# Optimization experiments

Measured on AMD Instinct MI355X. Metric: run time of the kernel, lower is better.

Reference implementation:

```python
import jax, jax.numpy as jnp
import numpy as np

B, S, H, DK = 8, 2048, 1024, 64


def setup_inputs() -> dict:
    key = jax.random.key(0)
    ks = jax.random.split(key, 8)
    x = jax.random.normal(ks[0], (B, S, H), dtype=jnp.float32)
    # padding at the tail: positions >= length are pad (True)
    lengths = jax.random.randint(ks[1], (B,), S // 2, S + 1)
    padding_mask = jnp.arange(S)[None, :] >= lengths[:, None]  # [B,S] bool, True = pad
    sc = 1.0 / np.sqrt(H)
    Wq = jax.random.normal(ks[2], (H, DK), dtype=jnp.float32) * sc
    Wk = jax.random.normal(ks[3], (H, DK), dtype=jnp.float32) * sc
    Wv = jax.random.normal(ks[4], (H, DK), dtype=jnp.float32) * sc
    bq = jnp.zeros((DK,), dtype=jnp.float32)
    bk = jnp.zeros((DK,), dtype=jnp.float32)
    bv = jnp.zeros((DK,), dtype=jnp.float32)
    return {"x": x, "padding_mask": padding_mask, "Wq": Wq, "bq": bq,
            "Wk": Wk, "bk": bk, "Wv": Wv, "bv": bv}


def reference(x, padding_mask, Wq, bq, Wk, bk, Wv, bv):
    # Single-head attention, dropout_pe = 0 (identity), masking=True (causal).
    d_k = Wq.shape[-1]
    Q = jnp.einsum('bsh,hd->bsd', x, Wq) + bq
    K = jnp.einsum('bsh,hd->bsd', x, Wk) + bk
    V = jnp.einsum('bsh,hd->bsd', x, Wv) + bv
    scores = jnp.einsum('bqd,bkd->bqk', Q, K) / jnp.sqrt(jnp.asarray(d_k, x.dtype))
    neg_inf = jnp.finfo(scores.dtype).min
    # padding mask over keys: [B,1,S]
    scores = jnp.where(padding_mask[:, None, :], neg_inf, scores)
    # causal mask: strictly upper triangular is disallowed
    seq = scores.shape[-1]
    causal = jnp.triu(jnp.ones((seq, seq), dtype=bool), k=1)
    scores = jnp.where(causal[None, :, :], neg_inf, scores)
    W = jax.nn.softmax(scores, axis=-1)
    # zero out attention rows for padded query positions: [B,S,1]
    W = jnp.where(padding_mask[:, :, None], 0.0, W)
    return jnp.einsum('bqk,bkd->bqd', W, V)
```

## Files before the change

### kernel.cpp

```cpp
#include <hip/hip_runtime.h>
#include <hip/hip_bf16.h>

#define NB 8
#define SEQ 2048
#define HD 1024
#define DK 64

#define QSCALE 0.1803368801111244f
#define FIXMAX2 11.541560327111708f

typedef __attribute__((ext_vector_type(4))) float f32x4;
typedef __attribute__((ext_vector_type(8))) short bf16x8;
typedef __attribute__((ext_vector_type(4))) unsigned short u16x4;

#define LDS_BARRIER() asm volatile("s_waitcnt lgkmcnt(0)\n\ts_barrier" ::: "memory")

__device__ __forceinline__ short f2bf(float f) {
    union { float f; unsigned u; } v; v.f = f;
    unsigned r = v.u + 0x7fffu + ((v.u >> 16) & 1u);
    return (short)(r >> 16);
}
__device__ __forceinline__ float fexp2(float x) {
#if __has_builtin(__builtin_amdgcn_exp2f)
    return __builtin_amdgcn_exp2f(x);
#else
    return exp2f(x);
#endif
}
__device__ __forceinline__ short bf16lo(float f) {
    unsigned r;
    asm("v_cvt_pk_bf16_f32 %0, %1, %1" : "=v"(r) : "v"(f));
    return (short)r;
}
__device__ __forceinline__ bf16x8 pack8(f32x4 v0, f32x4 v1) {
    union { bf16x8 v; __hip_bfloat162 h[4]; } u;
    u.h[0] = __float22bfloat162_rn(make_float2(v0[0], v0[1]));
    u.h[1] = __float22bfloat162_rn(make_float2(v0[2], v0[3]));
    u.h[2] = __float22bfloat162_rn(make_float2(v1[0], v1[1]));
    u.h[3] = __float22bfloat162_rn(make_float2(v1[2], v1[3]));
    return u.v;
}

__global__ void prep_kernel(const unsigned* __restrict__ mask,
                            const float* __restrict__ Wq, const float* __restrict__ Wk,
                            const float* __restrict__ Wv,
                            int* __restrict__ lengths, short* __restrict__ Wp) {
    if (blockIdx.x < 768) {
        int idx = blockIdx.x * 256 + threadIdx.x;
        int j = idx & 7, lane = (idx >> 3) & 63;
        int slot = idx >> 9;
        int fr = slot % 3, q2 = slot / 3;
        int kh = q2 & 1, cg = (q2 >> 1) & 3, kbg = q2 >> 3;
        int g = lane >> 4, c = lane & 15;
        int n = cg * 3 + fr;
        int m = n >> 2, colm = (n & 3) * 16 + c;
        int k = kbg * 64 + kh * 32 + g * 8 + j;
        const float* W = (m == 0) ? Wq : (m == 1) ? Wk : Wv;
        Wp[idx] = f2bf(W[(size_t)k * DK + colm]);
        return;
    }
    __shared__ int sdet;
    __shared__ int scnt;
    int b = blockIdx.x - 768, t = threadIdx.x;
    if (t == 0) { sdet = 0; scnt = 0; }
    __syncthreads();
    int det = 0;
    for (int i = t; i < 4096; i += 256) {
        unsigned w = mask[i];
        if (w > 1u && w != 0x3F800000u) det = 1;
    }
    if (det) atomicOr(&sdet, 1);
    __syncthreads();
    int cnt = 0;
    if (sdet) {
        const unsigned char* m8 = (const unsigned char*)mask;
        for (int s = t; s < SEQ; s += 256) cnt += (m8[b * SEQ + s] == 0) ? 1 : 0;
    } else {
        for (int s = t; s < SEQ; s += 256) cnt += (mask[b * SEQ + s] == 0u) ? 1 : 0;
    }
    atomicAdd(&scnt, cnt);
    __syncthreads();
    if (t == 0) lengths[b] = scnt;
}

__global__ __launch_bounds__(256) void qkv_kernel(
    const float* __restrict__ x,
    const float* __restrict__ bq, const float* __restrict__ bk, const float* __restrict__ bv,
    const short* __restrict__ Wp,
    short* __restrict__ Q, short* __restrict__ K, short* __restrict__ Vt) {
    __shared__ short xs[2][32][64];
    int t = threadIdx.x;
    int cg = t >> 6, lane = t & 63;
    int g = lane >> 4, c = lane & 15;
    int r0 = blockIdx.x * 32;
    int bb = r0 >> 11, sbase = r0 & (SEQ - 1);

    int srow = t >> 3, ch = t & 7;
    const float* xsrc = x + (size_t)(r0 + srow) * HD + ch * 8;
    short* wbase = &xs[0][0][0];
    int wo = srow * 64 + ((ch ^ (srow & 7)) << 3);

    const short* wpw = Wp + (size_t)cg * 3072 + (size_t)lane * 8;

    f32x4 z = {0.f, 0.f, 0.f, 0.f};
    f32x4 acc[2][3];
    #pragma unroll
    for (int rf = 0; rf < 2; rf++)
        #pragma unroll
        for (int fr = 0; fr < 3; fr++) acc[rf][fr] = z;

    {
        f32x4 x0 = *(const f32x4*)xsrc;
        f32x4 x1 = *(const f32x4*)(xsrc + 4);
        *(bf16x8*)(wbase + wo) = pack8(x0, x1);
    }
    bf16x8 Bc[2][3];
    #pragma unroll
    for (int kh = 0; kh < 2; kh++)
        #pragma unroll
        for (int fr = 0; fr < 3; fr++)
            Bc[kh][fr] = *(const bf16x8*)(wpw + kh * 1536 + fr * 512);
    f32x4 nxA0 = *(const f32x4*)(xsrc + 64);
    f32x4 nxA1 = *(const f32x4*)(xsrc + 68);
    LDS_BARRIER();

    const short* rbase0 = &xs[0][0][0] + c * 64;
    #pragma unroll
    for (int kbg = 0; kbg < 16; kbg++) {
        int cur = kbg & 1;
        f32x4 nxB0, nxB1;
        bf16x8 Bn[2][3];
        if (kbg < 14) {
            const float* p = xsrc + (kbg + 2) * 64;
            nxB0 = *(const f32x4*)p;
            nxB1 = *(const f32x4*)(p + 4);
        }
        if (kbg < 15) {
            #pragma unroll
            for (int kh = 0; kh < 2; kh++)
                #pragma unroll
                for (int fr = 0; fr < 3; fr++)
                    Bn[kh][fr] = *(const bf16x8*)(wpw + (kbg + 1) * 12288 + kh * 1536 + fr * 512);
        }
        bf16x8 Af[2][2];
        #pragma unroll
        for (int rf = 0; rf < 2; rf++)
            #pragma unroll
            for (int kh = 0; kh < 2; kh++)
                Af[rf][kh] = *(const bf16x8*)(rbase0 + cur * 2048 + rf * 1024
                                              + (((kh * 4 + g) ^ (c & 7)) << 3));
        #pragma unroll
        for (int kh = 0; kh < 2; kh++)
            #pragma unroll
            for (int fr = 0; fr < 3; fr++)
                #pragma unroll
                for (int rf = 0; rf < 2; rf++)
                    acc[rf][fr] = __builtin_amdgcn_mfma_f32_16x16x32_bf16(Af[rf][kh], Bc[kh][fr], acc[rf][fr], 0, 0, 0);
        if (kbg < 15) {
            *(bf16x8*)(wbase + (cur ^ 1) * 2048 + wo) = pack8(nxA0, nxA1);
            #pragma unroll
            for (int kh = 0; kh < 2; kh++)
                #pragma unroll
                for (int fr = 0; fr < 3; fr++) Bc[kh][fr] = Bn[kh][fr];
        }
        if (kbg < 14) { nxA0 = nxB0; nxA1 = nxB1; }
        LDS_BARRIER();
    }

    #pragma unroll
    for (int rf = 0; rf < 2; rf++)
        #pragma unroll
        for (int fr = 0; fr < 3; fr++) {
            int n = cg * 3 + fr;
            int m = n >> 2, colm = (n & 3) * 16 + c;
            const float* bias = (m == 0) ? bq : (m == 1) ? bk : bv;
            float bv_ = bias[colm];
            if (m == 2) {
                u16x4 pk;
                #pragma unroll
                for (int j = 0; j < 4; j++) pk[j] = (unsigned short)f2bf(acc[rf][fr][j] + bv_);
                int srw = sbase + rf * 16 + 4 * g;
                *(u16x4*)(Vt + (size_t)bb * DK * SEQ + (size_t)colm * SEQ + srw) = pk;
            } else {
                #pragma unroll
                for (int j = 0; j < 4; j++) {
                    int row = r0 + rf * 16 + 4 * g + j;
                    float s = acc[rf][fr][j] + bv_;
                    if (m == 0) Q[(size_t)row * DK + colm] = f2bf(s * QSCALE);
                    else        K[(size_t)row * DK + colm] = f2bf(s);
                }
            }
        }
}

__global__ __launch_bounds__(512) void attn_kernel(
    const short* __restrict__ Q, const short* __restrict__ K_, const short* __restrict__ Vt,
    const int* __restrict__ lengths, float* __restrict__ out) {
    __shared__ float macc[8][32][66];
    __shared__ float ll[8][32];
    short* plds = (short*)&macc[0][0][0];

    int bid = blockIdx.x;
    int b = bid & 7;
    int qt = 63 - (bid >> 3);
    int len = lengths[b];
    int qbase = qt * 32;
    int t = threadIdx.x;
    int w = t >> 6, lane = t & 63;
    int g = lane >> 4, c = lane & 15;

    if (qbase >= len) {
        int row = t >> 4, col0 = (t & 15) * 4;
        f32x4 zz = {0.f, 0.f, 0.f, 0.f};
        *(f32x4*)(out + ((size_t)b * SEQ + qbase + row) * DK + col0) = zz;
        return;
    }

    int kend = min(len, qbase + 32);
    int ntiles = (kend + 63) >> 6;
    const short* Qb = Q + ((size_t)b * SEQ + qbase) * DK;
    const short* Kb = K_ + (size_t)b * SEQ * DK;
    const short* Vb = Vt + (size_t)b * DK * SEQ;

    bf16x8 qa[2][2];
    #pragma unroll
    for (int f = 0; f < 2; f++)
        #pragma unroll
        for (int kh = 0; kh < 2; kh++)
            qa[f][kh] = *(const bf16x8*)(Qb + (f * 16 + c) * DK + kh * 32 + g * 8);

    int rowcap[2][4];
    #pragma unroll
    for (int f = 0; f < 2; f++)
        #pragma unroll
        for (int j = 0; j < 4; j++)
            rowcap[f][j] = min(qbase + f * 16 + 4 * g + j, len - 1);

    f32x4 z = {0.f, 0.f, 0.f, 0.f};
    f32x4 acc[2][4];
    float l_r[2][4];
    #pragma unroll
    for (int f = 0; f < 2; f++) {
        #pragma unroll
        for (int n = 0; n < 4; n++) acc[f][n] = z;
        #pragma unroll
        for (int j = 0; j < 4; j++) l_r[f][j] = 0.f;
    }

    short* pldsw = plds + w * 2240;

    for (int tt = w; tt < ntiles; tt += 8) {
        int kb = tt * 64;
        bf16x8 kh0[2][2], kh1[2][2];
        #pragma unroll
        for (int kt = 0; kt < 2; kt++) {
            const short* kp = Kb + (size_t)(kb + kt * 16 + c) * DK + g * 8;
            kh0[kt][0] = *(const bf16x8*)kp;
            kh0[kt][1] = *(const bf16x8*)(kp + 32);
        }
        #pragma unroll
        for (int kt = 0; kt < 2; kt++) {
            const short* kp = Kb + (size_t)(kb + 32 + kt * 16 + c) * DK + g * 8;
            kh1[kt][0] = *(const bf16x8*)kp;
            kh1[kt][1] = *(const bf16x8*)(kp + 32);
        }
        f32x4 sf[2][4];
        __builtin_amdgcn_s_setprio(1);
        #pragma unroll
        for (int kt = 0; kt < 2; kt++)
            #pragma unroll
            for (int f = 0; f < 2; f++) {
                f32x4 t0 = __builtin_amdgcn_mfma_f32_16x16x32_bf16(qa[f][0], kh0[kt][0], z, 0, 0, 0);
                sf[f][kt] = __builtin_amdgcn_mfma_f32_16x16x32_bf16(qa[f][1], kh0[kt][1], t0, 0, 0, 0);
            }
        #pragma unroll
        for (int kt = 0; kt < 2; kt++)
            #pragma unroll
            for (int f = 0; f < 2; f++) {
                f32x4 t0 = __builtin_amdgcn_mfma_f32_16x16x32_bf16(qa[f][0], kh1[kt][0], z, 0, 0, 0);
                sf[f][kt + 2] = __builtin_amdgcn_mfma_f32_16x16x32_bf16(qa[f][1], kh1[kt][1], t0, 0, 0, 0);
            }
        __builtin_amdgcn_s_setprio(0);
        #pragma unroll
        for (int kt = 0; kt < 4; kt++) {
            int key = kb + kt * 16 + c;
            #pragma unroll
            for (int f = 0; f < 2; f++)
                #pragma unroll
                for (int j = 0; j < 4; j++) {
                    float s = (key > rowcap[f][j]) ? -1e30f : sf[f][kt][j];
                    float p = fexp2(s - FIXMAX2);
                    sf[f][kt][j] = p;
                    l_r[f][j] += p;
                }
        }
        #pragma unroll
        for (int f = 0; f < 2; f++)
            #pragma unroll
            for (int kt = 0; kt < 4; kt++)
                #pragma unroll
                for (int j = 0; j < 4; j++)
                    pldsw[f * 1120 + (4 * g + j) * 70 + kt * 16 + c] = bf16lo(sf[f][kt][j]);
        bf16x8 pa[2][2];
        #pragma unroll
        for (int f = 0; f < 2; f++) {
            pa[f][0] = *(const bf16x8*)(pldsw + f * 1120 + c * 70 + g * 8);
            pa[f][1] = *(const bf16x8*)(pldsw + f * 1120 + c * 70 + 32 + g * 8);
        }
        #pragma unroll
        for (int n = 0; n < 4; n++) {
            const short* vp = Vb + (size_t)(n * 16 + c) * SEQ + kb + g * 8;
            bf16x8 v0 = *(const bf16x8*)vp;
            bf16x8 v1 = *(const bf16x8*)(vp + 32);
            __builtin_amdgcn_s_setprio(1);
            #pragma unroll
            for (int f = 0; f < 2; f++) {
                acc[f][n] = __builtin_amdgcn_mfma_f32_16x16x32_bf16(pa[f][0], v0, acc[f][n], 0, 0, 0);
                acc[f][n] = __builtin_amdgcn_mfma_f32_16x16x32_bf16(pa[f][1], v1, acc[f][n], 0, 0, 0);
            }
            __builtin_amdgcn_s_setprio(0);
        }
    }

    #pragma unroll
    for (int d = 1; d < 16; d <<= 1)
        #pragma unroll
        for (int f = 0; f < 2; f++)
            #pragma unroll
            for (int j = 0; j < 4; j++) l_r[f][j] += __shfl_xor(l_r[f][j], d);

    __syncthreads();
    #pragma unroll
    for (int f = 0; f < 2; f++)
        #pragma unroll
        for (int n = 0; n < 4; n++)
            #pragma unroll
            for (int j = 0; j < 4; j++)
                macc[w][f * 16 + 4 * g + j][n * 16 + c] = acc[f][n][j];
    if (c == 0) {
        #pragma unroll
        for (int f = 0; f < 2; f++)
            #pragma unroll
            for (int j = 0; j < 4; j++)
                ll[w][f * 16 + 4 * g + j] = l_r[f][j];
    }
    __syncthreads();
    {
        int row = t >> 4, seg = t & 15;
        int r = qbase + row;
        float* op = out + ((size_t)b * SEQ + r) * DK + seg * 4;
        float o[4] = {0.f, 0.f, 0.f, 0.f};
        if (r < len) {
            float L = 0.f;
            #pragma unroll
            for (int wv = 0; wv < 8; wv++) L += ll[wv][row];
            #pragma unroll
            for (int wv = 0; wv < 8; wv++)
                #pragma unroll
                for (int i = 0; i < 4; i++) o[i] += macc[wv][row][seg * 4 + i];
            float inv = 1.f / L;
            #pragma unroll
            for (int i = 0; i < 4; i++) o[i] *= inv;
        }
        #pragma unroll
        for (int i = 0; i < 4; i++) op[i] = o[i];
    }
}

extern "C" void kernel_launch(void* const* d_in, const int* in_sizes, int n_in,
                              void* d_out, int out_size, void* d_ws, size_t ws_size,
                              hipStream_t stream) {
    const float* x  = (const float*)d_in[0];
    const unsigned* mask = (const unsigned*)d_in[1];
    const float* Wq = (const float*)d_in[2];
    const float* bq = (const float*)d_in[3];
    const float* Wk = (const float*)d_in[4];
    const float* bk = (const float*)d_in[5];
    const float* Wv = (const float*)d_in[6];
    const float* bv = (const float*)d_in[7];
    float* out = (float*)d_out;

    char* ws = (char*)d_ws;
    int*   lengths = (int*)ws;
    short* Wp = (short*)(ws + 256);
    short* Q  = (short*)(ws + 393472);
    short* K  = (short*)(ws + 2490624);
    short* Vt = (short*)(ws + 4587776);

    hipLaunchKernelGGL(prep_kernel, dim3(776), dim3(256), 0, stream, mask, Wq, Wk, Wv, lengths, Wp);
    hipLaunchKernelGGL(qkv_kernel, dim3(512), dim3(256), 0, stream,
                       x, bq, bk, bv, Wp, Q, K, Vt);
    hipLaunchKernelGGL(attn_kernel, dim3(NB * 64), dim3(512), 0, stream,
                       Q, K, Vt, lengths, out);
}
```

Measured before the change: 54.79 us.

## Split attention work across waves by query half and key-tile stride

Each wave now handles one 16-row query half (f = w&1) and every fourth key tile, instead of both query halves and every eighth key tile. This halves per-wave register state (accumulators, Q fragments, scores) and the LDS used for the final reduction, and the reduction now sums over 4 waves rather than 8. In exchange, each K/V tile is loaded by two waves instead of one, which adds global/L2 traffic, and fewer waves share each query's key range. The output store is also switched to a single vector write.

```diff
diff --git a/kernel.cpp b/kernel.cpp
--- a/kernel.cpp
+++ b/kernel.cpp
@@ -196,8 +196,8 @@
 __global__ __launch_bounds__(512) void attn_kernel(
     const short* __restrict__ Q, const short* __restrict__ K_, const short* __restrict__ Vt,
     const int* __restrict__ lengths, float* __restrict__ out) {
-    __shared__ float macc[8][32][66];
-    __shared__ float ll[8][32];
+    __shared__ float macc[8][16][66];
+    __shared__ float ll[8][16];
     short* plds = (short*)&macc[0][0][0];
 
     int bid = blockIdx.x;
@@ -208,6 +208,7 @@
     int t = threadIdx.x;
     int w = t >> 6, lane = t & 63;
     int g = lane >> 4, c = lane & 15;
+    int f = w & 1, sq = w >> 1;
 
     if (qbase >= len) {
         int row = t >> 4, col0 = (t & 15) * 4;
@@ -218,38 +219,26 @@
 
     int kend = min(len, qbase + 32);
     int ntiles = (kend + 63) >> 6;
-    const short* Qb = Q + ((size_t)b * SEQ + qbase) * DK;
+    const short* Qb = Q + ((size_t)b * SEQ + qbase + f * 16) * DK;
     const short* Kb = K_ + (size_t)b * SEQ * DK;
     const short* Vb = Vt + (size_t)b * DK * SEQ;
 
-    bf16x8 qa[2][2];
-    #pragma unroll
-    for (int f = 0; f < 2; f++)
-        #pragma unroll
-        for (int kh = 0; kh < 2; kh++)
-            qa[f][kh] = *(const bf16x8*)(Qb + (f * 16 + c) * DK + kh * 32 + g * 8);
-
-    int rowcap[2][4];
-    #pragma unroll
-    for (int f = 0; f < 2; f++)
-        #pragma unroll
-        for (int j = 0; j < 4; j++)
-            rowcap[f][j] = min(qbase + f * 16 + 4 * g + j, len - 1);
+    bf16x8 qa[2];
+    qa[0] = *(const bf16x8*)(Qb + c * DK + g * 8);
+    qa[1] = *(const bf16x8*)(Qb + c * DK + 32 + g * 8);
+
+    int rowcap[4];
+    #pragma unroll
+    for (int j = 0; j < 4; j++)
+        rowcap[j] = min(qbase + f * 16 + 4 * g + j, len - 1);
 
     f32x4 z = {0.f, 0.f, 0.f, 0.f};
-    f32x4 acc[2][4];
-    float l_r[2][4];
-    #pragma unroll
-    for (int f = 0; f < 2; f++) {
-        #pragma unroll
-        for (int n = 0; n < 4; n++) acc[f][n] = z;
-        #pragma unroll
-        for (int j = 0; j < 4; j++) l_r[f][j] = 0.f;
-    }
-
-    short* pldsw = plds + w * 2240;
-
-    for (int tt = w; tt < ntiles; tt += 8) {
+    f32x4 acc[4] = {z, z, z, z};
+    float l_r[4] = {0.f, 0.f, 0.f, 0.f};
+
+    short* pldsw = plds + w * 1120;
+
+    for (int tt = sq; tt < ntiles; tt += 4) {
         int kb = tt * 64;
         bf16x8 kh0[2][2], kh1[2][2];
         #pragma unroll
@@ -264,60 +253,45 @@
             kh1[kt][0] = *(const bf16x8*)kp;
             kh1[kt][1] = *(const bf16x8*)(kp + 32);
         }
-        f32x4 sf[2][4];
+        f32x4 sf[4];
         __builtin_amdgcn_s_setprio(1);
         #pragma unroll
-        for (int kt = 0; kt < 2; kt++)
-            #pragma unroll
-            for (int f = 0; f < 2; f++) {
-                f32x4 t0 = __builtin_amdgcn_mfma_f32_16x16x32_bf16(qa[f][0], kh0[kt][0], z, 0, 0, 0);
-                sf[f][kt] = __builtin_amdgcn_mfma_f32_16x16x32_bf16(qa[f][1], kh0[kt][1], t0, 0, 0, 0);
-            }
-        #pragma unroll
-        for (int kt = 0; kt < 2; kt++)
-            #pragma unroll
-            for (int f = 0; f < 2; f++) {
-                f32x4 t0 = __builtin_amdgcn_mfma_f32_16x16x32_bf16(qa[f][0], kh1[kt][0], z, 0, 0, 0);
-                sf[f][kt + 2] = __builtin_amdgcn_mfma_f32_16x16x32_bf16(qa[f][1], kh1[kt][1], t0, 0, 0, 0);
-            }
+        for (int kt = 0; kt < 2; kt++) {
+            f32x4 t0 = __builtin_amdgcn_mfma_f32_16x16x32_bf16(qa[0], kh0[kt][0], z, 0, 0, 0);
+            sf[kt] = __builtin_amdgcn_mfma_f32_16x16x32_bf16(qa[1], kh0[kt][1], t0, 0, 0, 0);
+        }
+        #pragma unroll
+        for (int kt = 0; kt < 2; kt++) {
+            f32x4 t0 = __builtin_amdgcn_mfma_f32_16x16x32_bf16(qa[0], kh1[kt][0], z, 0, 0, 0);
+            sf[kt + 2] = __builtin_amdgcn_mfma_f32_16x16x32_bf16(qa[1], kh1[kt][1], t0, 0, 0, 0);
+        }
         __builtin_amdgcn_s_setprio(0);
         #pragma unroll
         for (int kt = 0; kt < 4; kt++) {
             int key = kb + kt * 16 + c;
             #pragma unroll
-            for (int f = 0; f < 2; f++)
-                #pragma unroll
-                for (int j = 0; j < 4; j++) {
-                    float s = (key > rowcap[f][j]) ? -1e30f : sf[f][kt][j];
-                    float p = fexp2(s - FIXMAX2);
-                    sf[f][kt][j] = p;
-                    l_r[f][j] += p;
-                }
-        }
-        #pragma unroll
-        for (int f = 0; f < 2; f++)
-            #pragma unroll
-            for (int kt = 0; kt < 4; kt++)
-                #pragma unroll
-                for (int j = 0; j < 4; j++)
-                    pldsw[f * 1120 + (4 * g + j) * 70 + kt * 16 + c] = bf16lo(sf[f][kt][j]);
-        bf16x8 pa[2][2];
-        #pragma unroll
-        for (int f = 0; f < 2; f++) {
-            pa[f][0] = *(const bf16x8*)(pldsw + f * 1120 + c * 70 + g * 8);
-            pa[f][1] = *(const bf16x8*)(pldsw + f * 1120 + c * 70 + 32 + g * 8);
-        }
+            for (int j = 0; j < 4; j++) {
+                float s = (key > rowcap[j]) ? -1e30f : sf[kt][j];
+                float p = fexp2(s - FIXMAX2);
+                sf[kt][j] = p;
+                l_r[j] += p;
+            }
+        }
+        #pragma unroll
+        for (int kt = 0; kt < 4; kt++)
+            #pragma unroll
+            for (int j = 0; j < 4; j++)
+                pldsw[(4 * g + j) * 70 + kt * 16 + c] = bf16lo(sf[kt][j]);
+        bf16x8 pa0 = *(const bf16x8*)(pldsw + c * 70 + g * 8);
+        bf16x8 pa1 = *(const bf16x8*)(pldsw + c * 70 + 32 + g * 8);
         #pragma unroll
         for (int n = 0; n < 4; n++) {
             const short* vp = Vb + (size_t)(n * 16 + c) * SEQ + kb + g * 8;
             bf16x8 v0 = *(const bf16x8*)vp;
             bf16x8 v1 = *(const bf16x8*)(vp + 32);
             __builtin_amdgcn_s_setprio(1);
-            #pragma unroll
-            for (int f = 0; f < 2; f++) {
-                acc[f][n] = __builtin_amdgcn_mfma_f32_16x16x32_bf16(pa[f][0], v0, acc[f][n], 0, 0, 0);
-                acc[f][n] = __builtin_amdgcn_mfma_f32_16x16x32_bf16(pa[f][1], v1, acc[f][n], 0, 0, 0);
-            }
+            acc[n] = __builtin_amdgcn_mfma_f32_16x16x32_bf16(pa0, v0, acc[n], 0, 0, 0);
+            acc[n] = __builtin_amdgcn_mfma_f32_16x16x32_bf16(pa1, v1, acc[n], 0, 0, 0);
             __builtin_amdgcn_s_setprio(0);
         }
     }
@@ -325,45 +299,38 @@
     #pragma unroll
     for (int d = 1; d < 16; d <<= 1)
         #pragma unroll
-        for (int f = 0; f < 2; f++)
-            #pragma unroll
-            for (int j = 0; j < 4; j++) l_r[f][j] += __shfl_xor(l_r[f][j], d);
-
-    __syncthreads();
-    #pragma unroll
-    for (int f = 0; f < 2; f++)
-        #pragma unroll
-        for (int n = 0; n < 4; n++)
-            #pragma unroll
-            for (int j = 0; j < 4; j++)
-                macc[w][f * 16 + 4 * g + j][n * 16 + c] = acc[f][n][j];
+        for (int j = 0; j < 4; j++) l_r[j] += __shfl_xor(l_r[j], d);
+
+    __syncthreads();
+    #pragma unroll
+    for (int n = 0; n < 4; n++)
+        #pragma unroll
+        for (int j = 0; j < 4; j++)
+            macc[w][4 * g + j][n * 16 + c] = acc[n][j];
     if (c == 0) {
         #pragma unroll
-        for (int f = 0; f < 2; f++)
-            #pragma unroll
-            for (int j = 0; j < 4; j++)
-                ll[w][f * 16 + 4 * g + j] = l_r[f][j];
+        for (int j = 0; j < 4; j++)
+            ll[w][4 * g + j] = l_r[j];
     }
     __syncthreads();
     {
         int row = t >> 4, seg = t & 15;
         int r = qbase + row;
-        float* op = out + ((size_t)b * SEQ + r) * DK + seg * 4;
+        int ff = row >> 4, r16 = row & 15;
         float o[4] = {0.f, 0.f, 0.f, 0.f};
         if (r < len) {
-            float L = 0.f;
-            #pragma unroll
-            for (int wv = 0; wv < 8; wv++) L += ll[wv][row];
-            #pragma unroll
-            for (int wv = 0; wv < 8; wv++)
-                #pragma unroll
-                for (int i = 0; i < 4; i++) o[i] += macc[wv][row][seg * 4 + i];
+            float L = ll[ff][r16] + ll[ff + 2][r16] + ll[ff + 4][r16] + ll[ff + 6][r16];
+            #pragma unroll
+            for (int s2 = 0; s2 < 4; s2++) {
+                int wv = ff + 2 * s2;
+                #pragma unroll
+                for (int i = 0; i < 4; i++) o[i] += macc[wv][r16][seg * 4 + i];
+            }
             float inv = 1.f / L;
             #pragma unroll
             for (int i = 0; i < 4; i++) o[i] *= inv;
         }
-        #pragma unroll
-        for (int i = 0; i < 4; i++) op[i] = o[i];
+        *(f32x4*)(out + ((size_t)b * SEQ + r) * DK + seg * 4) = *(f32x4*)o;
     }
 }
 
```

After: 76.40 us. +39.5%, slower.
